# Kernel optimization log

Hardware: AMD Instinct MI355X
Metric: run time of the kernel (lower is better)

The kernel has to match this reference:

```python
import jax, jax.numpy as jnp
import numpy as np

HID, CROSS, NBLK, HEADS = 1280, 768, 16, 8
HEAD_DIM = HID // HEADS
ATTN_SCALE = HEAD_DIM ** -0.5


def _cayley(P):
    # P: [g, b, b] unconstrained params -> block orthogonal Q via Cayley map
    A = P - jnp.swapaxes(P, -1, -2)              # skew-symmetric
    I = jnp.eye(P.shape[-1], dtype=P.dtype)
    return jnp.linalg.solve(I - A, I + A)        # (I-A)^{-1}(I+A), orthogonal


def _gsoft(x, P):
    # block-diagonal orthogonal transform: x [..., n], P [g, b, b], n = g*b
    g, b = P.shape[0], P.shape[1]
    Q = _cayley(P)
    xb = x.reshape(*x.shape[:-1], g, b)
    y = jnp.einsum('...gi,gij->...gj', xb, Q)
    return y.reshape(x.shape)


def _head_to_batch(x, B, H):
    # [B, S, H*d] -> [B*H, S, d]
    S = x.shape[1]
    return x.reshape(B, S, H, -1).transpose(0, 2, 1, 3).reshape(B * H, S, -1)


def _batch_to_head(x, B, H):
    # [B*H, S, d] -> [B, S, H*d]
    S = x.shape[1]
    return x.reshape(B, H, S, -1).transpose(0, 2, 1, 3).reshape(B, S, -1)


def setup_inputs() -> dict:
    key = jax.random.key(0)
    ks = jax.random.split(key, 24)
    bh, bc = HID // NBLK, CROSS // NBLK  # 80, 48
    d = {
        'hidden_states': jax.random.normal(ks[0], (8, 4096, HID), jnp.float32),
        'encoder_hidden_states': jax.random.normal(ks[1], (8, 77, CROSS), jnp.float32),
        'Pq_in': jax.random.normal(ks[2], (NBLK, bh, bh)) * 0.05,
        'Pk_in': jax.random.normal(ks[3], (NBLK, bc, bc)) * 0.05,
        'Pv_in': jax.random.normal(ks[4], (NBLK, bc, bc)) * 0.05,
        'Pout_in': jax.random.normal(ks[5], (NBLK, bh, bh)) * 0.05,
        'Pq_out': jax.random.normal(ks[6], (NBLK, bh, bh)) * 0.05,
        'Pk_out': jax.random.normal(ks[7], (NBLK, bh, bh)) * 0.05,
        'Pv_out': jax.random.normal(ks[8], (NBLK, bh, bh)) * 0.05,
        'Pout_out': jax.random.normal(ks[9], (NBLK, bh, bh)) * 0.05,
        'Wq': jax.random.normal(ks[10], (HID, HID)) * (HID ** -0.5),
        'Wk': jax.random.normal(ks[11], (HID, CROSS)) * (CROSS ** -0.5),
        'Wv': jax.random.normal(ks[12], (HID, CROSS)) * (CROSS ** -0.5),
        'Wout': jax.random.normal(ks[13], (HID, HID)) * (HID ** -0.5),
        'bout': jnp.zeros((HID,), jnp.float32),
        'q_scale': jnp.ones((HID,), jnp.float32),
        'k_scale': jnp.ones((HID,), jnp.float32),
        'v_scale': jnp.ones((HID,), jnp.float32),
        'out_scale': jnp.ones((HID,), jnp.float32),
    }
    return d


def reference(hidden_states, encoder_hidden_states, Pq_in, Pk_in, Pv_in, Pout_in,
              Pq_out, Pk_out, Pv_out, Pout_out, Wq, Wk, Wv, Wout, bout,
              q_scale, k_scale, v_scale, out_scale):
    B = hidden_states.shape[0]
    # Q path: gsoft -> linear -> gsoft -> scale
    q = _gsoft(hidden_states, Pq_in) @ Wq.T
    q = q_scale * _gsoft(q, Pq_out)
    # K, V paths on encoder states
    k = _gsoft(encoder_hidden_states, Pk_in) @ Wk.T
    k = k_scale * _gsoft(k, Pk_out)
    v = _gsoft(encoder_hidden_states, Pv_in) @ Wv.T
    v = v_scale * _gsoft(v, Pv_out)
    q = _head_to_batch(q, B, HEADS)   # [B*H, Sq, d]
    k = _head_to_batch(k, B, HEADS)   # [B*H, Sk, d]
    v = _head_to_batch(v, B, HEADS)
    scores = jnp.einsum('bqd,bkd->bqk', q, k) * ATTN_SCALE
    probs = jax.nn.softmax(scores, axis=-1)
    out = jnp.einsum('bqk,bkd->bqd', probs, v)
    out = _batch_to_head(out, B, HEADS)  # [B, Sq, HID]
    out = _gsoft(out, Pout_in) @ Wout.T  # linear without bias first
    out = out_scale * _gsoft(out, Pout_out)
    out = out + bout                     # bias added after gsoft+scale
    return out
```

## Files before the change

kernel.cpp:

```cpp
#include <hip/hip_runtime.h>

typedef __attribute__((ext_vector_type(4))) float f32x4;
typedef __attribute__((ext_vector_type(2))) float f32x2;
typedef __attribute__((ext_vector_type(8))) short short8;
typedef __attribute__((ext_vector_type(8))) __bf16 bf16x8;
typedef __attribute__((ext_vector_type(4))) unsigned short us4;

__device__ __forceinline__ unsigned short f2bf(float f) {
  unsigned u = __builtin_bit_cast(unsigned, f);
  u = (u + 0x7FFFu + ((u >> 16) & 1u)) >> 16;
  return (unsigned short)u;
}

__device__ __forceinline__ f32x4 mfma16(short8 a, short8 b, f32x4 c) {
  return __builtin_amdgcn_mfma_f32_16x16x32_bf16(
      __builtin_bit_cast(bf16x8, a), __builtin_bit_cast(bf16x8, b), c, 0, 0, 0);
}

__device__ __forceinline__ void gload16(const unsigned short* g, unsigned short* l) {
  __builtin_amdgcn_global_load_lds((const __attribute__((address_space(1))) void*)g,
                                   (__attribute__((address_space(3))) void*)l, 16, 0, 0);
}

__device__ __forceinline__ short8 ds_read128(unsigned off) {
  short8 r;
  asm volatile("ds_read_b128 %0, %1" : "=v"(r) : "v"(off));
  return r;
}

__device__ __forceinline__ f32x2 lo2(f32x4 v) { return __builtin_shufflevector(v, v, 0, 1); }
__device__ __forceinline__ f32x2 hi2(f32x4 v) { return __builtin_shufflevector(v, v, 2, 3); }

struct CayleyPtrs {
  const float* P[8];
  float* Q[8];
};

__launch_bounds__(256)
__global__ void front_kernel(CayleyPtrs ptrs, const float* __restrict__ hidden,
                             unsigned short* __restrict__ Xbf,
                             unsigned short* __restrict__ VbfT) {
  __shared__ float M[80 * 80];
  __shared__ float R[80 * 80];
  __shared__ float fcol[80];
  int bid = blockIdx.x, tid = threadIdx.x;

  if (bid < 128) {
    int t = bid >> 4, g = bid & 15;
    int n = (t < 6) ? 80 : 48;
    const float* Pg = ptrs.P[t] + (size_t)g * n * n;
    float* Qg = ptrs.Q[t] + (size_t)g * n * n;

    for (int idx = tid; idx < n * n; idx += 256) {
      int i = idx / n, j = idx - i * n;
      float a = Pg[i * n + j] - Pg[j * n + i];
      float id = (i == j) ? 1.0f : 0.0f;
      M[idx] = id - a;
      R[idx] = id + a;
    }
    __syncthreads();

    int nch = n >> 2;
    int tot = n * nch;
    for (int k = 0; k < n; ++k) {
      if (tid < n) {
        float inv = 1.0f / M[k * n + k];
        fcol[tid] = (tid == k) ? 0.0f : M[tid * n + k] * inv;
      }
      __syncthreads();
      for (int idx = tid; idx < tot; idx += 256) {
        int i = idx / nch, c = idx - i * nch;
        float f = fcol[i];
        ((f32x4*)&R[i * n])[c] = ((f32x4*)&R[i * n])[c] - f * ((const f32x4*)&R[k * n])[c];
      }
      int c0 = k >> 2, mw = nch - c0, totM = n * mw;
      for (int idx = tid; idx < totM; idx += 256) {
        int i = idx / mw, c = c0 + idx - i * mw;
        float f = fcol[i];
        ((f32x4*)&M[i * n])[c] = ((f32x4*)&M[i * n])[c] - f * ((const f32x4*)&M[k * n])[c];
      }
      __syncthreads();
    }
    for (int idx = tid; idx < n * n; idx += 256) {
      int i = idx / n;
      Qg[idx] = R[idx] / M[i * n + i];
    }
  } else if (bid < 2048) {
    long long nEl = 32768LL * 1280;
    long long i = ((long long)(bid - 128) * 256 + tid) * 4;
    long long stride = 1920LL * 256 * 4;
    for (; i < nEl; i += stride) {
      f32x4 v = *(const f32x4*)(hidden + i);
      us4 o;
      o[0] = f2bf(v[0]); o[1] = f2bf(v[1]); o[2] = f2bf(v[2]); o[3] = f2bf(v[3]);
      *(us4*)(Xbf + i) = o;
    }
  } else {
    long long nCh = 1280LL * 656 / 8;
    long long i = (long long)(bid - 2048) * 256 + tid;
    short8 zz = {0, 0, 0, 0, 0, 0, 0, 0};
    for (; i < nCh; i += 16LL * 256) *((short8*)VbfT + i) = zz;
  }
}

struct BuildArgs {
  const float* Qin[4];
  const float* W[4];
  const float* Qout[4];
  const float* scale[4];
  unsigned short* WeffT[4];
  float extra[4];
  int b[4];
  int Kin[4];
};

#define BS 84

__launch_bounds__(256)
__global__ void build_all(BuildArgs A) {
  __shared__ float Qs[80 * BS];
  __shared__ float Ws[80 * BS];
  __shared__ float T1[80 * BS];
  int z = blockIdx.z;
  int gi = blockIdx.x, go = blockIdx.y, tid = threadIdx.x;
  int b = A.b[z], Kin = A.Kin[z];
  float extra = A.extra[z];
  const float* Qin = A.Qin[z];
  const float* W = A.W[z];
  const float* Qout = A.Qout[z];
  const float* scale = A.scale[z];
  unsigned short* WeffT = A.WeffT[z];

  for (int idx = tid; idx < b * b; idx += 256) {
    int i = idx / b, j = idx - i * b;
    Qs[i * BS + j] = Qin[(size_t)gi * b * b + idx];
  }
  for (int idx = tid; idx < 80 * b; idx += 256) {
    int m = idx / b, j = idx - m * b;
    Ws[m * BS + j] = W[(size_t)(go * 80 + m) * Kin + gi * b + j];
  }
  __syncthreads();

  int itiles = b >> 2;
  int jch = b >> 2;
  int NT = itiles * 20;
  for (int t = tid; t < NT; t += 256) {
    int ti = t / 20, tm = t - ti * 20;
    int tmr = (tm >= jch) ? tm - jch : tm;
    f32x2 acc[4][4] = {};
    for (int jc0 = 0; jc0 < jch; ++jc0) {
      int jc = jc0 + tmr; if (jc >= jch) jc -= jch;
      f32x4 qa[4], wb[4];
#pragma unroll
      for (int p = 0; p < 4; ++p) qa[p] = *(const f32x4*)&Qs[(4 * ti + p) * BS + jc * 4];
#pragma unroll
      for (int p = 0; p < 4; ++p) wb[p] = *(const f32x4*)&Ws[(4 * tm + p) * BS + jc * 4];
#pragma unroll
      for (int p = 0; p < 4; ++p)
#pragma unroll
        for (int q = 0; q < 4; ++q)
          acc[p][q] += lo2(qa[p]) * lo2(wb[q]) + hi2(qa[p]) * hi2(wb[q]);
    }
#pragma unroll
    for (int p = 0; p < 4; ++p)
#pragma unroll
      for (int q = 0; q < 4; ++q)
        T1[(4 * ti + p) * BS + 4 * tm + q] = acc[p][q][0] + acc[p][q][1];
  }
  __syncthreads();
  for (int idx = tid; idx < 6400; idx += 256) {
    int m = idx / 80, n = idx - m * 80;
    Qs[n * BS + m] = Qout[(size_t)go * 6400 + idx];
  }
  __syncthreads();
  for (int t = tid; t < NT; t += 256) {
    int ti = t / 20, tn = t - ti * 20;
    f32x2 acc[4][4] = {};
    for (int mc0 = 0; mc0 < 20; ++mc0) {
      int mc = mc0 + tn; if (mc >= 20) mc -= 20;
      f32x4 ta[4], qb[4];
#pragma unroll
      for (int p = 0; p < 4; ++p) ta[p] = *(const f32x4*)&T1[(4 * ti + p) * BS + mc * 4];
#pragma unroll
      for (int p = 0; p < 4; ++p) qb[p] = *(const f32x4*)&Qs[(4 * tn + p) * BS + mc * 4];
#pragma unroll
      for (int p = 0; p < 4; ++p)
#pragma unroll
        for (int q = 0; q < 4; ++q)
          acc[p][q] += lo2(ta[p]) * lo2(qb[q]) + hi2(ta[p]) * hi2(qb[q]);
    }
#pragma unroll
    for (int q = 0; q < 4; ++q) {
      int col = go * 80 + 4 * tn + q;
      float sc = scale[col] * extra;
#pragma unroll
      for (int p = 0; p < 4; ++p)
        WeffT[(size_t)col * Kin + gi * b + 4 * ti + p] =
            f2bf((acc[p][q][0] + acc[p][q][1]) * sc);
    }
  }
}

template <bool CF32, bool BIAS>
__device__ __forceinline__ void gemm128_body(unsigned short* sh,
                                             const unsigned short* A,
                                             const unsigned short* Bt,
                                             void* Cp, const float* bias,
                                             int M, int N, int K, int nid) {
  unsigned short* As0 = sh;
  unsigned short* As1 = sh + 8192;
  unsigned short* Bs0 = sh + 16384;
  unsigned short* Bs1 = sh + 24576;
  int nbn = N >> 7;
  int bm = nid / nbn, bn = nid - bm * nbn;
  int row0 = bm << 7, col0 = bn << 7;

  int tid = threadIdx.x;
  int w = tid >> 6, l = tid & 63, lo = l & 15, hi = l >> 4;
  int wm = w >> 1, wn = w & 1;
  int rsw = lo & 7;

  int sr8 = l >> 3;
  int chunk = (l & 7) ^ sr8;
  const unsigned short* Ag = A + (size_t)(row0 + w * 32 + sr8) * K + chunk * 8;
  const unsigned short* Bg = Bt + (size_t)(col0 + w * 32 + sr8) * K + chunk * 8;

  unsigned a0b = (unsigned)(size_t)As0, a1b = (unsigned)(size_t)As1;
  unsigned b0b = (unsigned)(size_t)Bs0, b1b = (unsigned)(size_t)Bs1;

  int NT = K >> 6;

  f32x4 z = {0.0f, 0.0f, 0.0f, 0.0f};
  f32x4 acc[4][4];
#pragma unroll
  for (int m = 0; m < 4; ++m)
#pragma unroll
    for (int n = 0; n < 4; ++n) acc[m][n] = z;

  auto stage = [&](int t, unsigned short* la0, unsigned short* lb0) {
    const unsigned short* ag = Ag + t * 64;
    const unsigned short* bg = Bg + t * 64;
    unsigned short* la = la0 + w * 2048;
    unsigned short* lb = lb0 + w * 2048;
#pragma unroll
    for (int i = 0; i < 4; ++i) {
      gload16(ag + (size_t)(i * 8) * K, la + i * 512);
      gload16(bg + (size_t)(i * 8) * K, lb + i * 512);
    }
  };

  stage(0, As0, Bs0);
  stage(1, As1, Bs1);

  for (int t = 0; t < NT; ++t) {
    unsigned cAb = (t & 1) ? a1b : a0b;
    unsigned cBb = (t & 1) ? b1b : b0b;
    if (t == NT - 1) asm volatile("s_waitcnt vmcnt(0)" ::: "memory");
    else             asm volatile("s_waitcnt vmcnt(8)" ::: "memory");
    __builtin_amdgcn_s_barrier();
    __builtin_amdgcn_sched_barrier(0);

    short8 bf[4][2];
#pragma unroll
    for (int ni = 0; ni < 4; ++ni) {
      int col = wn * 64 + ni * 16 + lo;
#pragma unroll
      for (int kk = 0; kk < 2; ++kk)
        bf[ni][kk] = ds_read128(cBb + (unsigned)(col * 128 + (((kk * 4 + hi) ^ rsw) << 4)));
    }
#pragma unroll
    for (int mp = 0; mp < 2; ++mp) {
      short8 af[2][2];
#pragma unroll
      for (int mi = 0; mi < 2; ++mi) {
        int row = wm * 64 + (mp * 2 + mi) * 16 + lo;
#pragma unroll
        for (int kk = 0; kk < 2; ++kk)
          af[mi][kk] = ds_read128(cAb + (unsigned)(row * 128 + (((kk * 4 + hi) ^ rsw) << 4)));
      }
      asm volatile("s_waitcnt lgkmcnt(0)" ::: "memory");
      __builtin_amdgcn_sched_barrier(0);
      __builtin_amdgcn_s_setprio(1);
#pragma unroll
      for (int mi = 0; mi < 2; ++mi)
#pragma unroll
        for (int ni = 0; ni < 4; ++ni) {
          int m = mp * 2 + mi;
          acc[m][ni] = mfma16(af[mi][0], bf[ni][0], acc[m][ni]);
          acc[m][ni] = mfma16(af[mi][1], bf[ni][1], acc[m][ni]);
        }
      __builtin_amdgcn_s_setprio(0);
    }
    __builtin_amdgcn_sched_barrier(0);
    __builtin_amdgcn_s_barrier();
    if (t + 2 < NT) {
      if (t & 1) stage(t + 2, As1, Bs1);
      else       stage(t + 2, As0, Bs0);
    }
  }

#pragma unroll
  for (int m = 0; m < 4; ++m)
#pragma unroll
    for (int n = 0; n < 4; ++n) {
      int col = col0 + wn * 64 + n * 16 + lo;
#pragma unroll
      for (int j = 0; j < 4; ++j) {
        int row = row0 + wm * 64 + m * 16 + hi * 4 + j;
        float v = acc[m][n][j];
        if (BIAS) v += bias[col];
        if (CF32) ((float*)Cp)[(size_t)row * N + col] = v;
        else ((unsigned short*)Cp)[(size_t)row * N + col] = f2bf(v);
      }
    }
}

template <bool CF32, bool BIAS>
__launch_bounds__(256, 2)
__global__ void gemm128(const unsigned short* __restrict__ A,
                        const unsigned short* __restrict__ Bt,
                        void* __restrict__ Cp, const float* __restrict__ bias,
                        int M, int N, int K) {
  __shared__ alignas(128) unsigned short sh[4 * 8192];
  int per = gridDim.x >> 3;
  int nid = (blockIdx.x & 7) * per + (blockIdx.x >> 3);
  gemm128_body<CF32, BIAS>(sh, A, Bt, Cp, bias, M, N, K, nid);
}

__device__ __forceinline__ void kv_body(unsigned short* sh,
                                        const float* __restrict__ enc,
                                        const unsigned short* __restrict__ Bt,
                                        unsigned short* __restrict__ Kbf,
                                        unsigned short* __restrict__ VbfT,
                                        int bn, int bm, int z) {
  const int M = 616, N = 1280, K = 768;
  unsigned short* As = sh;
  unsigned short* Bs = sh + 5120;
  int tid = threadIdx.x;
  int l = tid & 63, wid = tid >> 6, lo = l & 15, hi = l >> 4;
  int wm = wid >> 1, wn = wid & 1;
  f32x4 zr = {0.0f, 0.0f, 0.0f, 0.0f};
  f32x4 acc[4][4];
#pragma unroll
  for (int m = 0; m < 4; ++m)
#pragma unroll
    for (int n = 0; n < 4; ++n) acc[m][n] = zr;
  int row0 = bm * 128;
  int ar = tid >> 2, acg = tid & 3;
  int bnr = tid >> 1, bhf = tid & 1;

  for (int k0 = 0; k0 < K; k0 += 32) {
    __syncthreads();
#pragma unroll
    for (int rr = 0; rr < 2; ++rr) {
      int row = ar + rr * 64;
      int grow = row0 + row;
      short8 v = {0, 0, 0, 0, 0, 0, 0, 0};
      if (grow < M) {
        const float* ap = enc + (size_t)grow * K + k0 + acg * 8;
        f32x4 v0 = *(const f32x4*)ap;
        f32x4 v1 = *(const f32x4*)(ap + 4);
        v[0] = (short)f2bf(v0[0]); v[1] = (short)f2bf(v0[1]);
        v[2] = (short)f2bf(v0[2]); v[3] = (short)f2bf(v0[3]);
        v[4] = (short)f2bf(v1[0]); v[5] = (short)f2bf(v1[1]);
        v[6] = (short)f2bf(v1[2]); v[7] = (short)f2bf(v1[3]);
      }
      *(short8*)&As[row * 40 + acg * 8] = v;
    }
    {
      const unsigned short* bp = Bt + (size_t)(bn * 128 + bnr) * K + k0 + bhf * 16;
      *(short8*)&Bs[bnr * 40 + bhf * 16] = *(const short8*)bp;
      *(short8*)&Bs[bnr * 40 + bhf * 16 + 8] = *(const short8*)(bp + 8);
    }
    __syncthreads();
    short8 af[4], bf[4];
#pragma unroll
    for (int m = 0; m < 4; ++m) af[m] = *(const short8*)&As[(wm * 64 + m * 16 + lo) * 40 + hi * 8];
#pragma unroll
    for (int n = 0; n < 4; ++n) bf[n] = *(const short8*)&Bs[(wn * 64 + n * 16 + lo) * 40 + hi * 8];
#pragma unroll
    for (int m = 0; m < 4; ++m)
#pragma unroll
      for (int n = 0; n < 4; ++n) acc[m][n] = mfma16(af[m], bf[n], acc[m][n]);
  }

#pragma unroll
  for (int m = 0; m < 4; ++m)
#pragma unroll
    for (int n = 0; n < 4; ++n) {
      int col = bn * 128 + wn * 64 + n * 16 + lo;
#pragma unroll
      for (int j = 0; j < 4; ++j) {
        int row = row0 + wm * 64 + m * 16 + hi * 4 + j;
        if (row < M) {
          unsigned short v = f2bf(acc[m][n][j]);
          if (z) {
            int bb = row / 77, tt = row - bb * 77;
            VbfT[(size_t)col * 656 + bb * 80 + tt] = v;
          } else {
            Kbf[(size_t)row * N + col] = v;
          }
        }
      }
    }
}

__launch_bounds__(256, 2)
__global__ void gemm_qkv(const unsigned short* __restrict__ Xbf,
                         const unsigned short* __restrict__ WqT,
                         unsigned short* __restrict__ Qbf,
                         const float* __restrict__ enc,
                         const unsigned short* __restrict__ WkT,
                         const unsigned short* __restrict__ WvT,
                         unsigned short* __restrict__ Kbf,
                         unsigned short* __restrict__ VbfT) {
  __shared__ alignas(128) unsigned short sh[4 * 8192];
  int bid = blockIdx.x;
  if (bid < 100) {
    int z = bid / 50, r = bid - z * 50;
    int bm = r / 10, bn = r - bm * 10;
    kv_body(sh, enc, z ? WvT : WkT, Kbf, VbfT, bn, bm, z);
  } else {
    int b2 = bid - 100;
    int nid = (b2 & 7) * 320 + (b2 >> 3);
    gemm128_body<false, false>(sh, Xbf, WqT, Qbf, nullptr, 32768, 1280, 1280, nid);
  }
}

#define QB 64
__launch_bounds__(256)
__global__ void attn_kernel(const unsigned short* __restrict__ Q,
                            const unsigned short* __restrict__ Kp,
                            const unsigned short* __restrict__ VpT,
                            unsigned short* __restrict__ O) {
  __shared__ alignas(16) unsigned short Ps[QB][104];
  int tile = blockIdx.x, bh = blockIdx.y;
  int b = bh >> 3, h = bh & 7;
  int tid = threadIdx.x;

  for (int cid = tid; cid < QB * 16; cid += 256) {
    int r = cid / 16, c = 80 + (cid & 15);
    Ps[r][c] = 0;
  }

  int l = tid & 63, wid = tid >> 6, lo = l & 15, hi = l >> 4;

  const unsigned short* qrow =
      Q + (size_t)(b * 4096 + tile * QB + wid * 16 + lo) * 1280 + h * 160;
  short8 a[5];
#pragma unroll
  for (int kt = 0; kt < 5; ++kt) a[kt] = *(const short8*)&qrow[kt * 32 + hi * 8];

  const unsigned short* Kb = Kp + (size_t)(b * 77) * 1280 + h * 160;
  f32x4 z = {0.0f, 0.0f, 0.0f, 0.0f};
  f32x4 sc[5];
#pragma unroll
  for (int n = 0; n < 5; ++n) sc[n] = z;
#pragma unroll
  for (int n = 0; n < 5; ++n) {
    const unsigned short* krow = Kb + (size_t)(n * 16 + lo) * 1280;
#pragma unroll
    for (int kt = 0; kt < 5; ++kt) {
      short8 bb = *(const short8*)&krow[kt * 32 + hi * 8];
      sc[n] = mfma16(a[kt], bb, sc[n]);
    }
  }
  if (lo >= 13) { sc[4][0] = -1e30f; sc[4][1] = -1e30f; sc[4][2] = -1e30f; sc[4][3] = -1e30f; }

  float pinv[4];
#pragma unroll
  for (int j = 0; j < 4; ++j) {
    float mx = sc[0][j];
#pragma unroll
    for (int n = 1; n < 5; ++n) mx = fmaxf(mx, sc[n][j]);
#pragma unroll
    for (int msk = 1; msk < 16; msk <<= 1) mx = fmaxf(mx, __shfl_xor(mx, msk, 64));
    float s = 0.0f;
#pragma unroll
    for (int n = 0; n < 5; ++n) {
      float p = __expf(sc[n][j] - mx);
      sc[n][j] = p;
      s += p;
    }
#pragma unroll
    for (int msk = 1; msk < 16; msk <<= 1) s += __shfl_xor(s, msk, 64);
    pinv[j] = 1.0f / s;
  }
#pragma unroll
  for (int n = 0; n < 5; ++n)
#pragma unroll
    for (int j = 0; j < 4; ++j)
      Ps[wid * 16 + hi * 4 + j][n * 16 + lo] = f2bf(sc[n][j] * pinv[j]);
  __syncthreads();

  f32x4 o[10];
#pragma unroll
  for (int n = 0; n < 10; ++n) o[n] = z;
#pragma unroll
  for (int kt = 0; kt < 3; ++kt) {
    short8 pa = *(const short8*)&Ps[wid * 16 + lo][kt * 32 + hi * 8];
#pragma unroll
    for (int n = 0; n < 10; ++n) {
      const unsigned short* vrow = VpT + (size_t)(h * 160 + n * 16 + lo) * 656 + b * 80;
      short8 vb = *(const short8*)&vrow[kt * 32 + hi * 8];
      o[n] = mfma16(pa, vb, o[n]);
    }
  }
  unsigned short* Ob = O + (size_t)(b * 4096 + tile * QB + wid * 16 + hi * 4) * 1280 + h * 160;
#pragma unroll
  for (int n = 0; n < 10; ++n)
#pragma unroll
    for (int j = 0; j < 4; ++j)
      Ob[(size_t)j * 1280 + n * 16 + lo] = f2bf(o[n][j]);
}

extern "C" void kernel_launch(void* const* d_in, const int* in_sizes, int n_in,
                              void* d_out, int out_size, void* d_ws, size_t ws_size,
                              hipStream_t stream) {
  const float* hidden   = (const float*)d_in[0];
  const float* enc      = (const float*)d_in[1];
  const float* Pq_in    = (const float*)d_in[2];
  const float* Pk_in    = (const float*)d_in[3];
  const float* Pv_in    = (const float*)d_in[4];
  const float* Pout_in  = (const float*)d_in[5];
  const float* Pq_out   = (const float*)d_in[6];
  const float* Pk_out   = (const float*)d_in[7];
  const float* Pv_out   = (const float*)d_in[8];
  const float* Pout_out = (const float*)d_in[9];
  const float* Wq       = (const float*)d_in[10];
  const float* Wk       = (const float*)d_in[11];
  const float* Wv       = (const float*)d_in[12];
  const float* Wout     = (const float*)d_in[13];
  const float* bout     = (const float*)d_in[14];
  const float* q_scale  = (const float*)d_in[15];
  const float* k_scale  = (const float*)d_in[16];
  const float* v_scale  = (const float*)d_in[17];
  const float* out_scale= (const float*)d_in[18];

  char* w = (char*)d_ws;
  unsigned short* attnO = (unsigned short*)w; w += 32768LL * 1280 * 2;
  unsigned short* WqT   = (unsigned short*)w; w += 1280LL * 1280 * 2;
  unsigned short* WkT   = (unsigned short*)w; w += 1280LL * 768 * 2;
  unsigned short* WvT   = (unsigned short*)w; w += 1280LL * 768 * 2;
  unsigned short* WoT   = (unsigned short*)w; w += 1280LL * 1280 * 2;
  unsigned short* Kbf   = (unsigned short*)w; w += 616LL * 1280 * 2;
  unsigned short* VbfT  = (unsigned short*)w; w += 1280LL * 656 * 2;
  float* cQq_in   = (float*)w; w += 16LL * 80 * 80 * 4;
  float* cQout_in = (float*)w; w += 16LL * 80 * 80 * 4;
  float* cQq_out  = (float*)w; w += 16LL * 80 * 80 * 4;
  float* cQk_out  = (float*)w; w += 16LL * 80 * 80 * 4;
  float* cQv_out  = (float*)w; w += 16LL * 80 * 80 * 4;
  float* cQout_out= (float*)w; w += 16LL * 80 * 80 * 4;
  float* cQk_in   = (float*)w; w += 16LL * 48 * 48 * 4;
  float* cQv_in   = (float*)w; w += 16LL * 48 * 48 * 4;

  unsigned short* Xbf = (unsigned short*)d_out;
  unsigned short* Qbf = Xbf + 32768LL * 1280;

  CayleyPtrs cp;
  cp.P[0] = Pq_in;    cp.Q[0] = cQq_in;
  cp.P[1] = Pout_in;  cp.Q[1] = cQout_in;
  cp.P[2] = Pq_out;   cp.Q[2] = cQq_out;
  cp.P[3] = Pk_out;   cp.Q[3] = cQk_out;
  cp.P[4] = Pv_out;   cp.Q[4] = cQv_out;
  cp.P[5] = Pout_out; cp.Q[5] = cQout_out;
  cp.P[6] = Pk_in;    cp.Q[6] = cQk_in;
  cp.P[7] = Pv_in;    cp.Q[7] = cQv_in;

  front_kernel<<<2064, 256, 0, stream>>>(cp, hidden, Xbf, VbfT);

  const float ATTN_SCALE = 0.07905694150420949f;
  BuildArgs ba;
  ba.Qin[0] = cQq_in;   ba.W[0] = Wq;   ba.Qout[0] = cQq_out;   ba.scale[0] = q_scale;
  ba.WeffT[0] = WqT;    ba.extra[0] = ATTN_SCALE; ba.b[0] = 80; ba.Kin[0] = 1280;
  ba.Qin[1] = cQk_in;   ba.W[1] = Wk;   ba.Qout[1] = cQk_out;   ba.scale[1] = k_scale;
  ba.WeffT[1] = WkT;    ba.extra[1] = 1.0f;       ba.b[1] = 48; ba.Kin[1] = 768;
  ba.Qin[2] = cQv_in;   ba.W[2] = Wv;   ba.Qout[2] = cQv_out;   ba.scale[2] = v_scale;
  ba.WeffT[2] = WvT;    ba.extra[2] = 1.0f;       ba.b[2] = 48; ba.Kin[2] = 768;
  ba.Qin[3] = cQout_in; ba.W[3] = Wout; ba.Qout[3] = cQout_out; ba.scale[3] = out_scale;
  ba.WeffT[3] = WoT;    ba.extra[3] = 1.0f;       ba.b[3] = 80; ba.Kin[3] = 1280;
  build_all<<<dim3(16, 16, 4), 256, 0, stream>>>(ba);

  gemm_qkv<<<2660, 256, 0, stream>>>(Xbf, WqT, Qbf, enc, WkT, WvT, Kbf, VbfT);
  attn_kernel<<<dim3(64, 64), 256, 0, stream>>>(Qbf, Kbf, VbfT, attnO);
  gemm128<true, true><<<2560, 256, 0, stream>>>(attnO, WoT, d_out, bout, 32768, 1280, 1280);
}
```

Before: 513.9 us.

## Fuse fp32-to-bf16 conversion of hidden states into Q GEMM A-tile loading

Removes the separate pass that converted the fp32 hidden states to a bf16 buffer in the front kernel. The Q projection GEMM now loads fp32 A tiles into registers, packs them to bf16 and writes them to LDS, pipelined one stage ahead, while B still uses direct global-to-LDS loads. This saves a full write and reread of a bf16 copy of the activations. In exchange the GEMM reads twice as many A bytes, uses more registers, and needs more complex waitcnt scheduling.

```diff
diff --git a/kernel.cpp b/kernel.cpp
--- a/kernel.cpp
+++ b/kernel.cpp
@@ -5,6 +5,7 @@
 typedef __attribute__((ext_vector_type(8))) short short8;
 typedef __attribute__((ext_vector_type(8))) __bf16 bf16x8;
 typedef __attribute__((ext_vector_type(4))) unsigned short us4;
+typedef __attribute__((ext_vector_type(4))) unsigned int u32x4;
 
 __device__ __forceinline__ unsigned short f2bf(float f) {
   unsigned u = __builtin_bit_cast(unsigned, f);
@@ -28,6 +29,22 @@
   return r;
 }
 
+__device__ __forceinline__ f32x4 gldf4(const float* p) {
+  f32x4 r;
+  asm volatile("global_load_dwordx4 %0, %1, off" : "=v"(r) : "v"(p) : "memory");
+  return r;
+}
+
+__device__ __forceinline__ unsigned cvtpk(float a, float b) {
+  unsigned r;
+  asm("v_cvt_pk_bf16_f32 %0, %1, %2" : "=v"(r) : "v"(a), "v"(b));
+  return r;
+}
+
+__device__ __forceinline__ void ds_write128(unsigned off, f32x4 d) {
+  asm volatile("ds_write_b128 %0, %1" :: "v"(off), "v"(d) : "memory");
+}
+
 __device__ __forceinline__ f32x2 lo2(f32x4 v) { return __builtin_shufflevector(v, v, 0, 1); }
 __device__ __forceinline__ f32x2 hi2(f32x4 v) { return __builtin_shufflevector(v, v, 2, 3); }
 
@@ -37,9 +54,7 @@
 };
 
 __launch_bounds__(256)
-__global__ void front_kernel(CayleyPtrs ptrs, const float* __restrict__ hidden,
-                             unsigned short* __restrict__ Xbf,
-                             unsigned short* __restrict__ VbfT) {
+__global__ void front_kernel(CayleyPtrs ptrs, unsigned short* __restrict__ VbfT) {
   __shared__ float M[80 * 80];
   __shared__ float R[80 * 80];
   __shared__ float fcol[80];
@@ -85,19 +100,9 @@
       int i = idx / n;
       Qg[idx] = R[idx] / M[i * n + i];
     }
-  } else if (bid < 2048) {
-    long long nEl = 32768LL * 1280;
-    long long i = ((long long)(bid - 128) * 256 + tid) * 4;
-    long long stride = 1920LL * 256 * 4;
-    for (; i < nEl; i += stride) {
-      f32x4 v = *(const f32x4*)(hidden + i);
-      us4 o;
-      o[0] = f2bf(v[0]); o[1] = f2bf(v[1]); o[2] = f2bf(v[2]); o[3] = f2bf(v[3]);
-      *(us4*)(Xbf + i) = o;
-    }
   } else {
     long long nCh = 1280LL * 656 / 8;
-    long long i = (long long)(bid - 2048) * 256 + tid;
+    long long i = (long long)(bid - 128) * 256 + tid;
     short8 zz = {0, 0, 0, 0, 0, 0, 0, 0};
     for (; i < nCh; i += 16LL * 256) *((short8*)VbfT + i) = zz;
   }
@@ -201,9 +206,9 @@
   }
 }
 
-template <bool CF32, bool BIAS>
+template <bool AF32, bool CF32, bool BIAS>
 __device__ __forceinline__ void gemm128_body(unsigned short* sh,
-                                             const unsigned short* A,
+                                             const void* Ap,
                                              const unsigned short* Bt,
                                              void* Cp, const float* bias,
                                              int M, int N, int K, int nid) {
@@ -222,11 +227,13 @@
 
   int sr8 = l >> 3;
   int chunk = (l & 7) ^ sr8;
-  const unsigned short* Ag = A + (size_t)(row0 + w * 32 + sr8) * K + chunk * 8;
+  const unsigned short* Agb = (const unsigned short*)Ap + (size_t)(row0 + w * 32 + sr8) * K + chunk * 8;
+  const float*          Agf = (const float*)Ap + (size_t)(row0 + w * 32 + sr8) * K + chunk * 8;
   const unsigned short* Bg = Bt + (size_t)(col0 + w * 32 + sr8) * K + chunk * 8;
 
   unsigned a0b = (unsigned)(size_t)As0, a1b = (unsigned)(size_t)As1;
   unsigned b0b = (unsigned)(size_t)Bs0, b1b = (unsigned)(size_t)Bs1;
+  unsigned awoff = (unsigned)((w * 32 + sr8) * 128 + (l & 7) * 16);
 
   int NT = K >> 6;
 
@@ -237,8 +244,14 @@
 #pragma unroll
     for (int n = 0; n < 4; ++n) acc[m][n] = z;
 
-  auto stage = [&](int t, unsigned short* la0, unsigned short* lb0) {
-    const unsigned short* ag = Ag + t * 64;
+  auto stageB = [&](int t, unsigned short* lb0) {
+    const unsigned short* bg = Bg + t * 64;
+    unsigned short* lb = lb0 + w * 2048;
+#pragma unroll
+    for (int i = 0; i < 4; ++i) gload16(bg + (size_t)(i * 8) * K, lb + i * 512);
+  };
+  auto stageFull = [&](int t, unsigned short* la0, unsigned short* lb0) {
+    const unsigned short* ag = Agb + t * 64;
     const unsigned short* bg = Bg + t * 64;
     unsigned short* la = la0 + w * 2048;
     unsigned short* lb = lb0 + w * 2048;
@@ -249,14 +262,56 @@
     }
   };
 
-  stage(0, As0, Bs0);
-  stage(1, As1, Bs1);
+  f32x4 aregs[8];
+  auto issueA = [&](int t) {
+    const float* p = Agf + t * 64;
+#pragma unroll
+    for (int i = 0; i < 4; ++i) {
+      aregs[2 * i]     = gldf4(p + (size_t)(i * 8) * K);
+      aregs[2 * i + 1] = gldf4(p + (size_t)(i * 8) * K + 4);
+    }
+  };
+  auto writeA = [&](unsigned abase) {
+#pragma unroll
+    for (int i = 0; i < 4; ++i) {
+      u32x4 d;
+      d[0] = cvtpk(aregs[2 * i][0], aregs[2 * i][1]);
+      d[1] = cvtpk(aregs[2 * i][2], aregs[2 * i][3]);
+      d[2] = cvtpk(aregs[2 * i + 1][0], aregs[2 * i + 1][1]);
+      d[3] = cvtpk(aregs[2 * i + 1][2], aregs[2 * i + 1][3]);
+      ds_write128(abase + awoff + (unsigned)(i * 1024), __builtin_bit_cast(f32x4, d));
+    }
+  };
+
+  if constexpr (AF32) {
+    issueA(0);
+    asm volatile("s_waitcnt vmcnt(0)" ::: "memory");
+    __builtin_amdgcn_sched_barrier(0);
+    writeA(a0b);
+    issueA(1);
+    stageB(0, Bs0);
+    asm volatile("s_waitcnt vmcnt(4)" ::: "memory");
+    __builtin_amdgcn_sched_barrier(0);
+    writeA(a1b);
+    asm volatile("s_waitcnt lgkmcnt(0)" ::: "memory");
+    issueA(2);
+    stageB(1, Bs1);
+  } else {
+    stageFull(0, As0, Bs0);
+    stageFull(1, As1, Bs1);
+  }
 
   for (int t = 0; t < NT; ++t) {
     unsigned cAb = (t & 1) ? a1b : a0b;
     unsigned cBb = (t & 1) ? b1b : b0b;
-    if (t == NT - 1) asm volatile("s_waitcnt vmcnt(0)" ::: "memory");
-    else             asm volatile("s_waitcnt vmcnt(8)" ::: "memory");
+    if constexpr (AF32) {
+      if (t + 2 < NT)      asm volatile("s_waitcnt vmcnt(12)" ::: "memory");
+      else if (t + 1 < NT) asm volatile("s_waitcnt vmcnt(4)" ::: "memory");
+      else                 asm volatile("s_waitcnt vmcnt(0)" ::: "memory");
+    } else {
+      if (t == NT - 1) asm volatile("s_waitcnt vmcnt(0)" ::: "memory");
+      else             asm volatile("s_waitcnt vmcnt(8)" ::: "memory");
+    }
     __builtin_amdgcn_s_barrier();
     __builtin_amdgcn_sched_barrier(0);
 
@@ -293,9 +348,20 @@
     }
     __builtin_amdgcn_sched_barrier(0);
     __builtin_amdgcn_s_barrier();
-    if (t + 2 < NT) {
-      if (t & 1) stage(t + 2, As1, Bs1);
-      else       stage(t + 2, As0, Bs0);
+    if constexpr (AF32) {
+      if (t + 2 < NT) {
+        asm volatile("s_waitcnt vmcnt(4)" ::: "memory");
+        __builtin_amdgcn_sched_barrier(0);
+        writeA((t & 1) ? a1b : a0b);
+        asm volatile("s_waitcnt lgkmcnt(0)" ::: "memory");
+        if (t + 3 < NT) issueA(t + 3);
+        stageB(t + 2, (t & 1) ? Bs1 : Bs0);
+      }
+    } else {
+      if (t + 2 < NT) {
+        if (t & 1) stageFull(t + 2, As1, Bs1);
+        else       stageFull(t + 2, As0, Bs0);
+      }
     }
   }
 
@@ -315,16 +381,16 @@
     }
 }
 
-template <bool CF32, bool BIAS>
+template <bool AF32, bool CF32, bool BIAS>
 __launch_bounds__(256, 2)
-__global__ void gemm128(const unsigned short* __restrict__ A,
+__global__ void gemm128(const void* __restrict__ A,
                         const unsigned short* __restrict__ Bt,
                         void* __restrict__ Cp, const float* __restrict__ bias,
                         int M, int N, int K) {
   __shared__ alignas(128) unsigned short sh[4 * 8192];
   int per = gridDim.x >> 3;
   int nid = (blockIdx.x & 7) * per + (blockIdx.x >> 3);
-  gemm128_body<CF32, BIAS>(sh, A, Bt, Cp, bias, M, N, K, nid);
+  gemm128_body<AF32, CF32, BIAS>(sh, A, Bt, Cp, bias, M, N, K, nid);
 }
 
 __device__ __forceinline__ void kv_body(unsigned short* sh,
@@ -406,7 +472,7 @@
 }
 
 __launch_bounds__(256, 2)
-__global__ void gemm_qkv(const unsigned short* __restrict__ Xbf,
+__global__ void gemm_qkv(const float* __restrict__ hidden,
                          const unsigned short* __restrict__ WqT,
                          unsigned short* __restrict__ Qbf,
                          const float* __restrict__ enc,
@@ -423,7 +489,7 @@
   } else {
     int b2 = bid - 100;
     int nid = (b2 & 7) * 320 + (b2 >> 3);
-    gemm128_body<false, false>(sh, Xbf, WqT, Qbf, nullptr, 32768, 1280, 1280, nid);
+    gemm128_body<true, false, false>(sh, hidden, WqT, Qbf, nullptr, 32768, 1280, 1280, nid);
   }
 }
 
@@ -554,8 +620,7 @@
   float* cQk_in   = (float*)w; w += 16LL * 48 * 48 * 4;
   float* cQv_in   = (float*)w; w += 16LL * 48 * 48 * 4;
 
-  unsigned short* Xbf = (unsigned short*)d_out;
-  unsigned short* Qbf = Xbf + 32768LL * 1280;
+  unsigned short* Qbf = (unsigned short*)d_out;
 
   CayleyPtrs cp;
   cp.P[0] = Pq_in;    cp.Q[0] = cQq_in;
@@ -567,7 +632,7 @@
   cp.P[6] = Pk_in;    cp.Q[6] = cQk_in;
   cp.P[7] = Pv_in;    cp.Q[7] = cQv_in;
 
-  front_kernel<<<2064, 256, 0, stream>>>(cp, hidden, Xbf, VbfT);
+  front_kernel<<<144, 256, 0, stream>>>(cp, VbfT);
 
   const float ATTN_SCALE = 0.07905694150420949f;
   BuildArgs ba;
@@ -581,7 +646,7 @@
   ba.WeffT[3] = WoT;    ba.extra[3] = 1.0f;       ba.b[3] = 80; ba.Kin[3] = 1280;
   build_all<<<dim3(16, 16, 4), 256, 0, stream>>>(ba);
 
-  gemm_qkv<<<2660, 256, 0, stream>>>(Xbf, WqT, Qbf, enc, WkT, WvT, Kbf, VbfT);
+  gemm_qkv<<<2660, 256, 0, stream>>>(hidden, WqT, Qbf, enc, WkT, WvT, Kbf, VbfT);
   attn_kernel<<<dim3(64, 64), 256, 0, stream>>>(Qbf, Kbf, VbfT, attnO);
-  gemm128<true, true><<<2560, 256, 0, stream>>>(attnO, WoT, d_out, bout, 32768, 1280, 1280);
-}
+  gemm128<false, true, true><<<2560, 256, 0, stream>>>(attnO, WoT, d_out, bout, 32768, 1280, 1280);
+}
```

Result: slower. 564.9 us (+9.9%).

## Halve GEMM K-tile to 32 and raise occupancy to four blocks per CU

Applied to the files above, without the earlier changes.

Shrinks the K-tile of the 128x128 GEMM body from 64 to 32, which halves LDS use per block (64KB to 32KB) and adjusts the XOR swizzle, load mapping and fragment reads to match. Launch bounds are raised to 4 blocks per CU so more waves can hide memory latency. The cost is twice as many barrier-synchronised iterations, each doing fewer MFMAs, and a tighter register budget that may cause spills with 64 accumulator floats per thread.

```diff
diff --git a/kernel.cpp b/kernel.cpp
--- a/kernel.cpp
+++ b/kernel.cpp
@@ -208,9 +208,9 @@
                                              void* Cp, const float* bias,
                                              int M, int N, int K, int nid) {
   unsigned short* As0 = sh;
-  unsigned short* As1 = sh + 8192;
-  unsigned short* Bs0 = sh + 16384;
-  unsigned short* Bs1 = sh + 24576;
+  unsigned short* As1 = sh + 4096;
+  unsigned short* Bs0 = sh + 8192;
+  unsigned short* Bs1 = sh + 12288;
   int nbn = N >> 7;
   int bm = nid / nbn, bn = nid - bm * nbn;
   int row0 = bm << 7, col0 = bn << 7;
@@ -218,17 +218,18 @@
   int tid = threadIdx.x;
   int w = tid >> 6, l = tid & 63, lo = l & 15, hi = l >> 4;
   int wm = w >> 1, wn = w & 1;
-  int rsw = lo & 7;
-
-  int sr8 = l >> 3;
-  int chunk = (l & 7) ^ sr8;
-  const unsigned short* Ag = A + (size_t)(row0 + w * 32 + sr8) * K + chunk * 8;
-  const unsigned short* Bg = Bt + (size_t)(col0 + w * 32 + sr8) * K + chunk * 8;
+  int rsw2 = (lo >> 1) & 3;
+  int slot = (hi ^ rsw2) << 4;
+
+  int sr = l >> 2;
+  int chunk = (l & 3) ^ ((l >> 3) & 3);
+  const unsigned short* Ag = A + (size_t)(row0 + w * 32 + sr) * K + chunk * 8;
+  const unsigned short* Bg = Bt + (size_t)(col0 + w * 32 + sr) * K + chunk * 8;
 
   unsigned a0b = (unsigned)(size_t)As0, a1b = (unsigned)(size_t)As1;
   unsigned b0b = (unsigned)(size_t)Bs0, b1b = (unsigned)(size_t)Bs1;
 
-  int NT = K >> 6;
+  int NT = K >> 5;
 
   f32x4 z = {0.0f, 0.0f, 0.0f, 0.0f};
   f32x4 acc[4][4];
@@ -238,15 +239,14 @@
     for (int n = 0; n < 4; ++n) acc[m][n] = z;
 
   auto stage = [&](int t, unsigned short* la0, unsigned short* lb0) {
-    const unsigned short* ag = Ag + t * 64;
-    const unsigned short* bg = Bg + t * 64;
-    unsigned short* la = la0 + w * 2048;
-    unsigned short* lb = lb0 + w * 2048;
-#pragma unroll
-    for (int i = 0; i < 4; ++i) {
-      gload16(ag + (size_t)(i * 8) * K, la + i * 512);
-      gload16(bg + (size_t)(i * 8) * K, lb + i * 512);
-    }
+    const unsigned short* ag = Ag + t * 32;
+    const unsigned short* bg = Bg + t * 32;
+    unsigned short* la = la0 + w * 1024;
+    unsigned short* lb = lb0 + w * 1024;
+    gload16(ag, la);
+    gload16(ag + (size_t)16 * K, la + 512);
+    gload16(bg, lb);
+    gload16(bg + (size_t)16 * K, lb + 512);
   };
 
   stage(0, As0, Bs0);
@@ -256,41 +256,28 @@
     unsigned cAb = (t & 1) ? a1b : a0b;
     unsigned cBb = (t & 1) ? b1b : b0b;
     if (t == NT - 1) asm volatile("s_waitcnt vmcnt(0)" ::: "memory");
-    else             asm volatile("s_waitcnt vmcnt(8)" ::: "memory");
+    else             asm volatile("s_waitcnt vmcnt(4)" ::: "memory");
     __builtin_amdgcn_s_barrier();
     __builtin_amdgcn_sched_barrier(0);
 
-    short8 bf[4][2];
-#pragma unroll
-    for (int ni = 0; ni < 4; ++ni) {
-      int col = wn * 64 + ni * 16 + lo;
-#pragma unroll
-      for (int kk = 0; kk < 2; ++kk)
-        bf[ni][kk] = ds_read128(cBb + (unsigned)(col * 128 + (((kk * 4 + hi) ^ rsw) << 4)));
-    }
-#pragma unroll
-    for (int mp = 0; mp < 2; ++mp) {
-      short8 af[2][2];
-#pragma unroll
-      for (int mi = 0; mi < 2; ++mi) {
-        int row = wm * 64 + (mp * 2 + mi) * 16 + lo;
-#pragma unroll
-        for (int kk = 0; kk < 2; ++kk)
-          af[mi][kk] = ds_read128(cAb + (unsigned)(row * 128 + (((kk * 4 + hi) ^ rsw) << 4)));
-      }
-      asm volatile("s_waitcnt lgkmcnt(0)" ::: "memory");
-      __builtin_amdgcn_sched_barrier(0);
-      __builtin_amdgcn_s_setprio(1);
-#pragma unroll
-      for (int mi = 0; mi < 2; ++mi)
-#pragma unroll
-        for (int ni = 0; ni < 4; ++ni) {
-          int m = mp * 2 + mi;
-          acc[m][ni] = mfma16(af[mi][0], bf[ni][0], acc[m][ni]);
-          acc[m][ni] = mfma16(af[mi][1], bf[ni][1], acc[m][ni]);
-        }
-      __builtin_amdgcn_s_setprio(0);
-    }
+    short8 bf[4], af[4];
+#pragma unroll
+    for (int ni = 0; ni < 4; ++ni)
+      bf[ni] = ds_read128(cBb + (unsigned)((wn * 64 + ni * 16 + lo) * 64 + slot));
+#pragma unroll
+    for (int mi = 0; mi < 4; ++mi)
+      af[mi] = ds_read128(cAb + (unsigned)((wm * 64 + mi * 16 + lo) * 64 + slot));
+
+    asm volatile("s_waitcnt lgkmcnt(0)" ::: "memory");
+    __builtin_amdgcn_sched_barrier(0);
+    __builtin_amdgcn_s_setprio(1);
+#pragma unroll
+    for (int mi = 0; mi < 4; ++mi)
+#pragma unroll
+      for (int ni = 0; ni < 4; ++ni)
+        acc[mi][ni] = mfma16(af[mi], bf[ni], acc[mi][ni]);
+    __builtin_amdgcn_s_setprio(0);
+
     __builtin_amdgcn_sched_barrier(0);
     __builtin_amdgcn_s_barrier();
     if (t + 2 < NT) {
@@ -316,12 +303,12 @@
 }
 
 template <bool CF32, bool BIAS>
-__launch_bounds__(256, 2)
+__launch_bounds__(256, 4)
 __global__ void gemm128(const unsigned short* __restrict__ A,
                         const unsigned short* __restrict__ Bt,
                         void* __restrict__ Cp, const float* __restrict__ bias,
                         int M, int N, int K) {
-  __shared__ alignas(128) unsigned short sh[4 * 8192];
+  __shared__ alignas(128) unsigned short sh[16384];
   int per = gridDim.x >> 3;
   int nid = (blockIdx.x & 7) * per + (blockIdx.x >> 3);
   gemm128_body<CF32, BIAS>(sh, A, Bt, Cp, bias, M, N, K, nid);
@@ -405,7 +392,7 @@
     }
 }
 
-__launch_bounds__(256, 2)
+__launch_bounds__(256, 4)
 __global__ void gemm_qkv(const unsigned short* __restrict__ Xbf,
                          const unsigned short* __restrict__ WqT,
                          unsigned short* __restrict__ Qbf,
@@ -414,7 +401,7 @@
                          const unsigned short* __restrict__ WvT,
                          unsigned short* __restrict__ Kbf,
                          unsigned short* __restrict__ VbfT) {
-  __shared__ alignas(128) unsigned short sh[4 * 8192];
+  __shared__ alignas(128) unsigned short sh[16384];
   int bid = blockIdx.x;
   if (bid < 100) {
     int z = bid / 50, r = bid - z * 50;
```

New measurement: 534.0 us. 3.9% more time.
